# Performance work log

Hardware: AMD Instinct MI355X
Metric: run time of the kernel (lower is better)

The kernel has to match this reference:

```python
import jax, jax.numpy as jnp
import numpy as np

NUM_ITERATIONS = 3


def squash(v, axis=-1):
    sq = jnp.sum(v * v, axis=axis, keepdims=True)
    scale = sq / (1.0 + sq)
    return scale * v / jnp.sqrt(sq)


def setup_inputs() -> dict:
    key = jax.random.key(0)
    k1, k2 = jax.random.split(key)
    B, N, IN, OUT, CAPS = 512, 4608, 16, 32, 32
    x = jax.random.normal(k1, (B, N, IN), dtype=jnp.float32)
    # torch.rand -> uniform [0, 1)
    route_weights = jax.random.uniform(k2, (N, IN, OUT), dtype=jnp.float32)
    return {"x": x, "route_weights": route_weights, "num_capsules": CAPS}


def reference(x, route_weights, num_capsules):
    # x: [B, N, IN], route_weights: [N, IN, OUT]
    u_hat = jnp.einsum('bnk,nkl->bnl', x, route_weights)  # [B, N, OUT]
    N = x.shape[1]
    b = jnp.zeros((N, num_capsules), dtype=u_hat.dtype)  # routing logits [N, CAPS]
    v = None
    for it in range(NUM_ITERATIONS):
        c = jax.nn.softmax(b, axis=-1)                     # [N, CAPS]
        s = jnp.einsum('bnk,nc->bck', u_hat, c)            # [B, CAPS, OUT]
        v = squash(s, axis=-1)                             # [B, CAPS, OUT]
        if it < NUM_ITERATIONS - 1:
            b = b + jnp.einsum('bnk,bck->nc', u_hat, v)    # agreement, reduced over batch
    return v
```

## Files before the change

kernel.cpp:

```cpp
#include <hip/hip_runtime.h>


#define NB 512
#define KTOT 73728
#define OUTC 32
#define NCAPS 32

#define KSPLIT 64
#define KCHUNK (KTOT / KSPLIT)
#define KT 128
#define NTILES (KCHUNK / KT)
#define NQ (KT / 4)
#define RPW 2
#define NWAVES 4
#define RPB (NWAVES * 2 * RPW)
#define NRG (NB / RPB)
#define KSTR (KT + 4)

#define WS_NEED ((size_t)KSPLIT * NB * OUTC * 4)

__global__ __launch_bounds__(256) void zero_ws(float* __restrict__ S) {
    int i = blockIdx.x * 256 + threadIdx.x;
    if (i < NB * OUTC) S[i] = 0.0f;
}

template <bool PART>
__global__ __launch_bounds__(256) void gemm_k(
        const float* __restrict__ x, const float* __restrict__ w,
        float* __restrict__ S) {
    __shared__ float wlds[OUTC * KSTR];
    const int t = threadIdx.x;
    const int lane = t & 63;
    const int l32 = lane & 31;
    const int half = lane >> 5;
    const int wave = t >> 6;
    const int bx = blockIdx.x, by = blockIdx.y;
    const int row0 = bx * RPB + wave * (2 * RPW) + half * RPW;
    const size_t kbase = (size_t)by * KCHUNK;

    const int sc = t & 31;
    const int sh = t >> 5;

    float acc[RPW][OUTC];
#pragma unroll
    for (int r = 0; r < RPW; ++r)
#pragma unroll
        for (int c = 0; c < OUTC; ++c) acc[r][c] = 0.0f;

    const float4* xq[RPW];
#pragma unroll
    for (int r = 0; r < RPW; ++r)
        xq[r] = (const float4*)(x + (size_t)(row0 + r) * KTOT + kbase);

    for (int tile = 0; tile < NTILES; ++tile) {
        float4 xv[RPW];
#pragma unroll
        for (int r = 0; r < RPW; ++r)
            xv[r] = xq[r][tile * NQ + l32];

#pragma unroll
        for (int jj = 0; jj < 4; ++jj) {
            int kq = jj * 8 + sh;
            int kk = 4 * kq;
            const float* wg = w + (kbase + (size_t)tile * KT + kk) * OUTC + sc;
            float w0 = wg[0];
            float w1 = wg[OUTC];
            float w2 = wg[2 * OUTC];
            float w3 = wg[3 * OUTC];
            *(float4*)&wlds[sc * KSTR + kk] = make_float4(w0, w1, w2, w3);
        }
        __syncthreads();

#pragma unroll
        for (int c = 0; c < OUTC; ++c) {
            float4 wv = *(const float4*)&wlds[c * KSTR + 4 * l32];
#pragma unroll
            for (int r = 0; r < RPW; ++r) {
                float a = acc[r][c];
                a = fmaf(xv[r].x, wv.x, a);
                a = fmaf(xv[r].y, wv.y, a);
                a = fmaf(xv[r].z, wv.z, a);
                a = fmaf(xv[r].w, wv.w, a);
                acc[r][c] = a;
            }
        }
        __syncthreads();
    }

#pragma unroll
    for (int r = 0; r < RPW; ++r) {
        float myv = 0.0f;
#pragma unroll
        for (int c = 0; c < OUTC; ++c) {
            float v = acc[r][c];
            v += __shfl_xor(v, 16, 64);
            v += __shfl_xor(v, 8, 64);
            v += __shfl_xor(v, 4, 64);
            v += __shfl_xor(v, 2, 64);
            v += __shfl_xor(v, 1, 64);
            if (l32 == c) myv = v;
        }
        const int row = row0 + r;
        if (PART)
            S[((size_t)by * NB + row) * OUTC + l32] = myv;
        else
            atomicAdd(&S[(size_t)row * OUTC + l32], myv);
    }
}

template <bool PART>
__global__ __launch_bounds__(64) void finalize_k(const float* __restrict__ S,
                                                 float* __restrict__ out) {
    const int b = blockIdx.x;
    const int t = threadIdx.x;
    const int k = t & 31;
    const int h = t >> 5;
    float s;
    if (PART) {
        float a = 0.0f;
#pragma unroll
        for (int i = 0; i < KSPLIT / 2; ++i)
            a += S[((size_t)(h * (KSPLIT / 2) + i) * NB + b) * OUTC + k];
        a += __shfl_xor(a, 32, 64);
        s = a * (1.0f / 32.0f);
    } else {
        s = S[(size_t)b * OUTC + k] * (1.0f / 32.0f);
    }
    float sq = s * s;
    sq += __shfl_xor(sq, 16, 64);
    sq += __shfl_xor(sq, 8, 64);
    sq += __shfl_xor(sq, 4, 64);
    sq += __shfl_xor(sq, 2, 64);
    sq += __shfl_xor(sq, 1, 64);
    float scale = sq / ((1.0f + sq) * sqrtf(sq));
    float v = s * scale;
    float* orow = out + (size_t)b * (NCAPS * OUTC);
#pragma unroll
    for (int j = 0; j < 16; ++j)
        orow[(h + j * 2) * OUTC + k] = v;
}

extern "C" void kernel_launch(void* const* d_in, const int* in_sizes, int n_in,
                              void* d_out, int out_size, void* d_ws, size_t ws_size,
                              hipStream_t stream) {
    const float* x = (const float*)d_in[0];
    const float* w = (const float*)d_in[1];
    float* out = (float*)d_out;
    float* S = (float*)d_ws;

    if (ws_size >= WS_NEED) {
        hipLaunchKernelGGL((gemm_k<true>), dim3(NRG, KSPLIT), dim3(256), 0, stream,
                           x, w, S);
        hipLaunchKernelGGL((finalize_k<true>), dim3(NB), dim3(64), 0, stream, S, out);
    } else {
        hipLaunchKernelGGL(zero_ws, dim3((NB * OUTC + 255) / 256), dim3(256), 0,
                           stream, S);
        hipLaunchKernelGGL((gemm_k<false>), dim3(NRG, KSPLIT), dim3(256), 0, stream,
                           x, w, S);
        hipLaunchKernelGGL((finalize_k<false>), dim3(NB), dim3(64), 0, stream, S, out);
    }
}
```

Measured before the change: 279.3 us.

## Replace FP32 FMA GEMM with bf16 MFMA using pre-swizzled weight layout

Adds a prep kernel that converts route weights to bf16 in an MFMA-fragment layout. The main reduction now runs on 16x16x32 bf16 MFMA instructions, with x converted to bf16 on the fly and the K dimension split twice as finely. The aim is to move the large x·W reduction off scalar FMAs and LDS staging so it becomes bound by streaming x from memory. Rounding to bf16 costs accuracy, and a workspace-size fallback keeps the old FP32 path.

```diff
diff --git a/kernel.cpp b/kernel.cpp
--- a/kernel.cpp
+++ b/kernel.cpp
@@ -6,106 +6,96 @@
 #define OUTC 32
 #define NCAPS 32
 
-#define KSPLIT 64
+#define KSPLIT 128
 #define KCHUNK (KTOT / KSPLIT)
-#define KT 128
-#define NTILES (KCHUNK / KT)
-#define NQ (KT / 4)
-#define RPW 2
-#define NWAVES 4
-#define RPB (NWAVES * 2 * RPW)
-#define NRG (NB / RPB)
-#define KSTR (KT + 4)
-
-#define WS_NEED ((size_t)KSPLIT * NB * OUTC * 4)
-
-__global__ __launch_bounds__(256) void zero_ws(float* __restrict__ S) {
+#define NSTEP (KCHUNK / 32)
+#define NSTEPS_TOT (KTOT / 32)
+#define WT_BYTES ((size_t)NSTEPS_TOT * 2 * 64 * 8 * 2)
+#define SPA_BYTES ((size_t)KSPLIT * NB * OUTC * 4)
+#define S_BYTES ((size_t)NB * OUTC * 4)
+
+typedef short bf16x8 __attribute__((ext_vector_type(8)));
+typedef float f32x4 __attribute__((ext_vector_type(4)));
+
+__device__ __forceinline__ unsigned int f2bf(float f) {
+    union { float f; unsigned int u; } v; v.f = f;
+    unsigned int u = v.u;
+    return (u + 0x7fffu + ((u >> 16) & 1u)) >> 16;
+}
+
+__global__ __launch_bounds__(256) void wt_prep(const float* __restrict__ w,
+                                               unsigned short* __restrict__ wt) {
+    int tt = blockIdx.x * 256 + threadIdx.x;
+    int lane = tt & 63;
+    int h = (tt >> 6) & 1;
+    int step = tt >> 7;
+    int k0 = step * 32 + ((lane >> 4) & 3) * 8;
+    int c = h * 16 + (lane & 15);
+    const float* wp = w + (size_t)k0 * OUTC + c;
+    unsigned int u[4];
+#pragma unroll
+    for (int j = 0; j < 4; ++j) {
+        unsigned int lo = f2bf(wp[(2 * j) * OUTC]);
+        unsigned int hi = f2bf(wp[(2 * j + 1) * OUTC]);
+        u[j] = lo | (hi << 16);
+    }
+    *(uint4*)(wt + (size_t)tt * 8) = make_uint4(u[0], u[1], u[2], u[3]);
+}
+
+template <bool PART>
+__global__ __launch_bounds__(256) void gemm_mfma(
+        const float* __restrict__ x, const unsigned short* __restrict__ wt,
+        float* __restrict__ S) {
+    const int t = threadIdx.x;
+    const int lane = t & 63;
+    const int wave = t >> 6;
+    const int bx = blockIdx.x;
+    const int by = blockIdx.y;
+    const int row0 = by * 64 + wave * 16;
+    const int m = lane & 15;
+    const int q = lane >> 4;
+    const size_t kbase = (size_t)bx * KCHUNK;
+
+    const float* xp = x + (size_t)(row0 + m) * KTOT + kbase + q * 8;
+    const unsigned short* wp = wt + (kbase >> 5) * 1024 + lane * 8;
+
+    f32x4 acc0 = {0.f, 0.f, 0.f, 0.f};
+    f32x4 acc1 = {0.f, 0.f, 0.f, 0.f};
+
+#pragma unroll 6
+    for (int s = 0; s < NSTEP; ++s) {
+        float4 xa = *(const float4*)xp;
+        float4 xb = *(const float4*)(xp + 4);
+        xp += 32;
+        bf16x8 b0 = *(const bf16x8*)(wp);
+        bf16x8 b1 = *(const bf16x8*)(wp + 512);
+        wp += 1024;
+        bf16x8 a;
+        a[0] = (short)f2bf(xa.x); a[1] = (short)f2bf(xa.y);
+        a[2] = (short)f2bf(xa.z); a[3] = (short)f2bf(xa.w);
+        a[4] = (short)f2bf(xb.x); a[5] = (short)f2bf(xb.y);
+        a[6] = (short)f2bf(xb.z); a[7] = (short)f2bf(xb.w);
+        acc0 = __builtin_amdgcn_mfma_f32_16x16x32_bf16(a, b0, acc0, 0, 0, 0);
+        acc1 = __builtin_amdgcn_mfma_f32_16x16x32_bf16(a, b1, acc1, 0, 0, 0);
+    }
+
+#pragma unroll
+    for (int r = 0; r < 4; ++r) {
+        const int row = row0 + q * 4 + r;
+        if (PART) {
+            float* dst = S + ((size_t)bx * NB + row) * OUTC;
+            dst[m] = acc0[r];
+            dst[16 + m] = acc1[r];
+        } else {
+            atomicAdd(&S[(size_t)row * OUTC + m], acc0[r]);
+            atomicAdd(&S[(size_t)row * OUTC + 16 + m], acc1[r]);
+        }
+    }
+}
+
+__global__ __launch_bounds__(256) void zero_s(float* __restrict__ S) {
     int i = blockIdx.x * 256 + threadIdx.x;
     if (i < NB * OUTC) S[i] = 0.0f;
-}
-
-template <bool PART>
-__global__ __launch_bounds__(256) void gemm_k(
-        const float* __restrict__ x, const float* __restrict__ w,
-        float* __restrict__ S) {
-    __shared__ float wlds[OUTC * KSTR];
-    const int t = threadIdx.x;
-    const int lane = t & 63;
-    const int l32 = lane & 31;
-    const int half = lane >> 5;
-    const int wave = t >> 6;
-    const int bx = blockIdx.x, by = blockIdx.y;
-    const int row0 = bx * RPB + wave * (2 * RPW) + half * RPW;
-    const size_t kbase = (size_t)by * KCHUNK;
-
-    const int sc = t & 31;
-    const int sh = t >> 5;
-
-    float acc[RPW][OUTC];
-#pragma unroll
-    for (int r = 0; r < RPW; ++r)
-#pragma unroll
-        for (int c = 0; c < OUTC; ++c) acc[r][c] = 0.0f;
-
-    const float4* xq[RPW];
-#pragma unroll
-    for (int r = 0; r < RPW; ++r)
-        xq[r] = (const float4*)(x + (size_t)(row0 + r) * KTOT + kbase);
-
-    for (int tile = 0; tile < NTILES; ++tile) {
-        float4 xv[RPW];
-#pragma unroll
-        for (int r = 0; r < RPW; ++r)
-            xv[r] = xq[r][tile * NQ + l32];
-
-#pragma unroll
-        for (int jj = 0; jj < 4; ++jj) {
-            int kq = jj * 8 + sh;
-            int kk = 4 * kq;
-            const float* wg = w + (kbase + (size_t)tile * KT + kk) * OUTC + sc;
-            float w0 = wg[0];
-            float w1 = wg[OUTC];
-            float w2 = wg[2 * OUTC];
-            float w3 = wg[3 * OUTC];
-            *(float4*)&wlds[sc * KSTR + kk] = make_float4(w0, w1, w2, w3);
-        }
-        __syncthreads();
-
-#pragma unroll
-        for (int c = 0; c < OUTC; ++c) {
-            float4 wv = *(const float4*)&wlds[c * KSTR + 4 * l32];
-#pragma unroll
-            for (int r = 0; r < RPW; ++r) {
-                float a = acc[r][c];
-                a = fmaf(xv[r].x, wv.x, a);
-                a = fmaf(xv[r].y, wv.y, a);
-                a = fmaf(xv[r].z, wv.z, a);
-                a = fmaf(xv[r].w, wv.w, a);
-                acc[r][c] = a;
-            }
-        }
-        __syncthreads();
-    }
-
-#pragma unroll
-    for (int r = 0; r < RPW; ++r) {
-        float myv = 0.0f;
-#pragma unroll
-        for (int c = 0; c < OUTC; ++c) {
-            float v = acc[r][c];
-            v += __shfl_xor(v, 16, 64);
-            v += __shfl_xor(v, 8, 64);
-            v += __shfl_xor(v, 4, 64);
-            v += __shfl_xor(v, 2, 64);
-            v += __shfl_xor(v, 1, 64);
-            if (l32 == c) myv = v;
-        }
-        const int row = row0 + r;
-        if (PART)
-            S[((size_t)by * NB + row) * OUTC + l32] = myv;
-        else
-            atomicAdd(&S[(size_t)row * OUTC + l32], myv);
-    }
 }
 
 template <bool PART>
@@ -118,7 +108,7 @@
     float s;
     if (PART) {
         float a = 0.0f;
-#pragma unroll
+#pragma unroll 8
         for (int i = 0; i < KSPLIT / 2; ++i)
             a += S[((size_t)(h * (KSPLIT / 2) + i) * NB + b) * OUTC + k];
         a += __shfl_xor(a, 32, 64);
@@ -140,23 +130,117 @@
         orow[(h + j * 2) * OUTC + k] = v;
 }
 
+#define FKSPLIT 64
+#define FKCHUNK 1152
+#define FKT 128
+#define FNQ 32
+#define FRPW 2
+#define FKSTR 132
+
+__global__ __launch_bounds__(256) void gemm_fb(
+        const float* __restrict__ x, const float* __restrict__ w,
+        float* __restrict__ S) {
+    __shared__ float wlds[OUTC * FKSTR];
+    const int t = threadIdx.x;
+    const int lane = t & 63;
+    const int l32 = lane & 31;
+    const int half = lane >> 5;
+    const int wave = t >> 6;
+    const int row0 = blockIdx.x * 16 + wave * 4 + half * FRPW;
+    const size_t kbase = (size_t)blockIdx.y * FKCHUNK;
+    const int sc = t & 31;
+    const int sh = t >> 5;
+
+    float acc[FRPW][OUTC];
+#pragma unroll
+    for (int r = 0; r < FRPW; ++r)
+#pragma unroll
+        for (int c = 0; c < OUTC; ++c) acc[r][c] = 0.0f;
+
+    const float4* xq[FRPW];
+#pragma unroll
+    for (int r = 0; r < FRPW; ++r)
+        xq[r] = (const float4*)(x + (size_t)(row0 + r) * KTOT + kbase);
+
+    for (int tile = 0; tile < FKCHUNK / FKT; ++tile) {
+        float4 xv[FRPW];
+#pragma unroll
+        for (int r = 0; r < FRPW; ++r)
+            xv[r] = xq[r][tile * FNQ + l32];
+#pragma unroll
+        for (int jj = 0; jj < 4; ++jj) {
+            int kk = 4 * (jj * 8 + sh);
+            const float* wg = w + (kbase + (size_t)tile * FKT + kk) * OUTC + sc;
+            *(float4*)&wlds[sc * FKSTR + kk] =
+                make_float4(wg[0], wg[OUTC], wg[2 * OUTC], wg[3 * OUTC]);
+        }
+        __syncthreads();
+#pragma unroll
+        for (int c = 0; c < OUTC; ++c) {
+            float4 wv = *(const float4*)&wlds[c * FKSTR + 4 * l32];
+#pragma unroll
+            for (int r = 0; r < FRPW; ++r) {
+                float a = acc[r][c];
+                a = fmaf(xv[r].x, wv.x, a);
+                a = fmaf(xv[r].y, wv.y, a);
+                a = fmaf(xv[r].z, wv.z, a);
+                a = fmaf(xv[r].w, wv.w, a);
+                acc[r][c] = a;
+            }
+        }
+        __syncthreads();
+    }
+#pragma unroll
+    for (int r = 0; r < FRPW; ++r) {
+        float myv = 0.0f;
+#pragma unroll
+        for (int c = 0; c < OUTC; ++c) {
+            float v = acc[r][c];
+            v += __shfl_xor(v, 16, 64);
+            v += __shfl_xor(v, 8, 64);
+            v += __shfl_xor(v, 4, 64);
+            v += __shfl_xor(v, 2, 64);
+            v += __shfl_xor(v, 1, 64);
+            if (l32 == c) myv = v;
+        }
+        atomicAdd(&S[(size_t)(row0 + r) * OUTC + l32], myv);
+    }
+}
+
 extern "C" void kernel_launch(void* const* d_in, const int* in_sizes, int n_in,
                               void* d_out, int out_size, void* d_ws, size_t ws_size,
                               hipStream_t stream) {
     const float* x = (const float*)d_in[0];
     const float* w = (const float*)d_in[1];
     float* out = (float*)d_out;
-    float* S = (float*)d_ws;
-
-    if (ws_size >= WS_NEED) {
-        hipLaunchKernelGGL((gemm_k<true>), dim3(NRG, KSPLIT), dim3(256), 0, stream,
+
+    if (ws_size >= WT_BYTES + SPA_BYTES) {
+        unsigned short* wt = (unsigned short*)d_ws;
+        float* S = (float*)((char*)d_ws + WT_BYTES);
+        hipLaunchKernelGGL(wt_prep, dim3(NSTEPS_TOT * 128 / 256), dim3(256), 0,
+                           stream, w, wt);
+        hipLaunchKernelGGL((gemm_mfma<true>), dim3(KSPLIT, 8), dim3(256), 0,
+                           stream, x, wt, S);
+        hipLaunchKernelGGL((finalize_k<true>), dim3(NB), dim3(64), 0, stream,
+                           S, out);
+    } else if (ws_size >= WT_BYTES + S_BYTES) {
+        unsigned short* wt = (unsigned short*)d_ws;
+        float* S = (float*)((char*)d_ws + WT_BYTES);
+        hipLaunchKernelGGL(wt_prep, dim3(NSTEPS_TOT * 128 / 256), dim3(256), 0,
+                           stream, w, wt);
+        hipLaunchKernelGGL(zero_s, dim3((NB * OUTC + 255) / 256), dim3(256), 0,
+                           stream, S);
+        hipLaunchKernelGGL((gemm_mfma<false>), dim3(KSPLIT, 8), dim3(256), 0,
+                           stream, x, wt, S);
+        hipLaunchKernelGGL((finalize_k<false>), dim3(NB), dim3(64), 0, stream,
+                           S, out);
+    } else {
+        float* S = (float*)d_ws;
+        hipLaunchKernelGGL(zero_s, dim3((NB * OUTC + 255) / 256), dim3(256), 0,
+                           stream, S);
+        hipLaunchKernelGGL(gemm_fb, dim3(32, FKSPLIT), dim3(256), 0, stream,
                            x, w, S);
-        hipLaunchKernelGGL((finalize_k<true>), dim3(NB), dim3(64), 0, stream, S, out);
-    } else {
-        hipLaunchKernelGGL(zero_ws, dim3((NB * OUTC + 255) / 256), dim3(256), 0,
-                           stream, S);
-        hipLaunchKernelGGL((gemm_k<false>), dim3(NRG, KSPLIT), dim3(256), 0, stream,
-                           x, w, S);
-        hipLaunchKernelGGL((finalize_k<false>), dim3(NB), dim3(64), 0, stream, S, out);
-    }
-}
+        hipLaunchKernelGGL((finalize_k<false>), dim3(NB), dim3(64), 0, stream,
+                           S, out);
+    }
+}
```

New measurement: 226.3 us. 1.23x faster.
